# Performance work log

Hardware: AMD Instinct MI355X
Metric: run time of the kernel (lower is better)

The kernel has to match this reference:

```python
import jax, jax.numpy as jnp
import numpy as np

N_NODES = 50000


def _gcn_layer(x, src, dst, norm_src, norm_dst, W, b, act):
    # DGL GraphConv with norm='both': D_out^{-1/2} A D_in^{-1/2} X W + b
    h = x * norm_src[:, None]                      # scale by src out-degree
    m = h[src]                                     # gather messages [E, d]
    agg = jax.ops.segment_sum(m, dst, num_segments=N_NODES)  # scatter-add
    agg = agg * norm_dst[:, None]
    out = agg @ W + b
    if act:
        out = jax.nn.relu(out)
    return out


def setup_inputs() -> dict:
    key = jax.random.key(0)
    ks = jax.random.split(key, 10)
    E = 800000
    in_size, hid, out_size = 128, 128, 64
    features = jax.random.normal(ks[0], (N_NODES, in_size), dtype=jnp.float32)
    src = jax.random.randint(ks[1], (E,), 0, N_NODES, dtype=jnp.int32)
    dst = jax.random.randint(ks[2], (E,), 0, N_NODES, dtype=jnp.int32)
    s = 0.05
    W1 = jax.random.normal(ks[3], (in_size, hid), dtype=jnp.float32) * s
    b1 = jnp.zeros((hid,), dtype=jnp.float32)
    W2 = jax.random.normal(ks[4], (hid, hid), dtype=jnp.float32) * s
    b2 = jnp.zeros((hid,), dtype=jnp.float32)
    W3 = jax.random.normal(ks[5], (hid, out_size), dtype=jnp.float32) * s
    b3 = jnp.zeros((out_size,), dtype=jnp.float32)
    return {"features": features, "W1": W1, "b1": b1, "W2": W2, "b2": b2,
            "W3": W3, "b3": b3, "src": src, "dst": dst}


def reference(features, W1, b1, W2, b2, W3, b3, src, dst):
    ones = jnp.ones(src.shape, dtype=features.dtype)
    out_deg = jax.ops.segment_sum(ones, src, num_segments=N_NODES)
    in_deg = jax.ops.segment_sum(ones, dst, num_segments=N_NODES)
    norm_src = jnp.maximum(out_deg, 1.0) ** -0.5   # clamp(min=1) as in DGL
    norm_dst = jnp.maximum(in_deg, 1.0) ** -0.5
    h = _gcn_layer(features, src, dst, norm_src, norm_dst, W1, b1, act=True)
    # dropout is identity in eval mode
    h = _gcn_layer(h, src, dst, norm_src, norm_dst, W2, b2, act=True)
    h = _gcn_layer(h, src, dst, norm_src, norm_dst, W3, b3, act=False)
    return h
```

## Files before the change

kernel.cpp:

```cpp
#include <hip/hip_runtime.h>
#include <math.h>

#define N_NODES 50000
#define K_DIM 128
#define CAP 64

typedef __attribute__((ext_vector_type(8))) short short8_t;
typedef __attribute__((ext_vector_type(4))) float f32x4_t;
typedef __attribute__((ext_vector_type(8))) _Float16 half8_t;

__device__ inline unsigned short f2bf(float x) {
    unsigned u = __float_as_uint(x);
    unsigned r = u + 0x7fffu + ((u >> 16) & 1u);
    return (unsigned short)(r >> 16);
}
__device__ inline float bf2f(unsigned short h) {
    return __uint_as_float(((unsigned)h) << 16);
}

__global__ __launch_bounds__(256) void prep_kernel(unsigned* __restrict__ cur,
                                                   unsigned* __restrict__ cnt_out,
                                                   _Float16* Yx, _Float16* Yy, _Float16* Yz) {
    int i = blockIdx.x * 256 + threadIdx.x;
    if (i < N_NODES) { cur[i] = 0u; cnt_out[i] = 0u; }
    if (blockIdx.x == 0) {
        int t = threadIdx.x;
        if (t < 128) {
            Yx[(size_t)N_NODES * 128 + t] = (_Float16)0.f;
            Yy[(size_t)N_NODES * 128 + t] = (_Float16)0.f;
        }
        if (t < 64) Yz[(size_t)N_NODES * 64 + t] = (_Float16)0.f;
    }
}

__global__ __launch_bounds__(256) void scatter_count_kernel(const int* __restrict__ src,
                                                            const int* __restrict__ dst, int E,
                                                            unsigned* __restrict__ cnt_out,
                                                            unsigned* __restrict__ cur,
                                                            int* __restrict__ csr) {
    int i = blockIdx.x * 256 + threadIdx.x;
    if (i >= E) return;
    int s = src[i], d = dst[i];
    atomicAdd(&cnt_out[s], 1u);
    unsigned p = atomicAdd(&cur[d], 1u);
    if (p < CAP) csr[((size_t)d << 6) + p] = s;
}

__global__ __launch_bounds__(256) void finalize_kernel(
        const unsigned* __restrict__ cur, const unsigned* __restrict__ cnt_out,
        int* __restrict__ indeg, float* __restrict__ nsrc, float* __restrict__ ndst,
        const float* __restrict__ W1, const float* __restrict__ W2,
        const float* __restrict__ W3,
        unsigned short* __restrict__ W1h, unsigned short* __restrict__ W1l,
        unsigned short* __restrict__ W2h, unsigned short* __restrict__ W2l,
        unsigned short* __restrict__ W3h, unsigned short* __restrict__ W3l) {
    if (blockIdx.x < 196) {
        int v = blockIdx.x * 256 + threadIdx.x;
        if (v >= N_NODES) return;
        unsigned id = cur[v];
        unsigned od = cnt_out[v];
        indeg[v] = (int)(id < CAP ? id : CAP);
        unsigned odc = od < 1u ? 1u : od;
        unsigned idc = id < 1u ? 1u : id;
        nsrc[v] = 1.0f / sqrtf((float)odc);
        ndst[v] = 1.0f / sqrtf((float)idc);
        return;
    }
    int gi = (blockIdx.x - 196) * 256 + threadIdx.x;
    const float* W; unsigned short *WBh, *WBl; int M, i;
    if (gi < 2048)      { W = W1; WBh = W1h; WBl = W1l; M = 128; i = gi; }
    else if (gi < 4096) { W = W2; WBh = W2h; WBl = W2l; M = 128; i = gi - 2048; }
    else if (gi < 5120) { W = W3; WBh = W3h; WBl = W3l; M = 64;  i = gi - 4096; }
    else return;
    int c    = i >> 8;
    int rem  = i & 255;
    int kc   = rem >> 6;
    int lane = rem & 63;
    int m = lane & 15, q = lane >> 4;
    int n = c * 16 + m;
    #pragma unroll
    for (int j = 0; j < 8; ++j) {
        int k = kc * 32 + q * 8 + j;
        float w = W[(size_t)k * M + n];
        unsigned short hi = f2bf(w);
        unsigned short lo = f2bf(w - bf2f(hi));
        WBh[(size_t)i * 8 + j] = hi;
        WBl[(size_t)i * 8 + j] = lo;
    }
}

template <int M>
__global__ __launch_bounds__(256) void gemm_mfma_kernel(
        const float* __restrict__ X,
        const unsigned short* __restrict__ WBh_,
        const unsigned short* __restrict__ WBl_,
        const float* __restrict__ nsrc, _Float16* __restrict__ Yh, int n) {
    constexpr int LSTR = 136;
    __shared__ short Xhi[64 * LSTR];
    __shared__ short Xlo[64 * LSTR];
    int tid = threadIdx.x;
    int lane = tid & 63, wave = tid >> 6;
    int rowBlock = blockIdx.x * 64;

    #pragma unroll
    for (int l = 0; l < 8; ++l) {
        int idx = (tid + l * 256) * 4;
        int r = idx >> 7;
        int c = idx & 127;
        float4 v = make_float4(0.f, 0.f, 0.f, 0.f);
        int gr = rowBlock + r;
        if (gr < n) v = *(const float4*)&X[(size_t)gr * K_DIM + c];
        unsigned short h0 = f2bf(v.x), h1 = f2bf(v.y), h2 = f2bf(v.z), h3 = f2bf(v.w);
        short4 hs = {(short)h0, (short)h1, (short)h2, (short)h3};
        short4 ls = {(short)f2bf(v.x - bf2f(h0)), (short)f2bf(v.y - bf2f(h1)),
                     (short)f2bf(v.z - bf2f(h2)), (short)f2bf(v.w - bf2f(h3))};
        *(short4*)&Xhi[r * LSTR + c] = hs;
        *(short4*)&Xlo[r * LSTR + c] = ls;
    }
    __syncthreads();

    int m = lane & 15, q = lane >> 4;
    short8_t ah[4], al[4];
    {
        int abase = (wave * 16 + m) * LSTR + q * 8;
        #pragma unroll
        for (int kc = 0; kc < 4; ++kc) {
            ah[kc] = *(const short8_t*)&Xhi[abase + kc * 32];
            al[kc] = *(const short8_t*)&Xlo[abase + kc * 32];
        }
    }
    float ns[4];
    int orow0 = rowBlock + wave * 16 + q * 4;
    #pragma unroll
    for (int r = 0; r < 4; ++r) ns[r] = (orow0 + r < n) ? nsrc[orow0 + r] : 0.f;

    const short8_t* WBh = (const short8_t*)WBh_;
    const short8_t* WBl = (const short8_t*)WBl_;
    constexpr int CT = M / 16;
    #pragma unroll
    for (int c = 0; c < CT; ++c) {
        short8_t bh[4], bl[4];
        #pragma unroll
        for (int kc = 0; kc < 4; ++kc) {
            bh[kc] = WBh[(c * 4 + kc) * 64 + lane];
            bl[kc] = WBl[(c * 4 + kc) * 64 + lane];
        }
        f32x4_t acc = {0.f, 0.f, 0.f, 0.f};
        #pragma unroll
        for (int kc = 0; kc < 4; ++kc) {
            acc = __builtin_amdgcn_mfma_f32_16x16x32_bf16(ah[kc], bh[kc], acc, 0, 0, 0);
            acc = __builtin_amdgcn_mfma_f32_16x16x32_bf16(ah[kc], bl[kc], acc, 0, 0, 0);
            acc = __builtin_amdgcn_mfma_f32_16x16x32_bf16(al[kc], bh[kc], acc, 0, 0, 0);
        }
        int col = c * 16 + m;
        #pragma unroll
        for (int r = 0; r < 4; ++r) {
            int row = orow0 + r;
            if (row < n) Yh[(size_t)row * M + col] = (_Float16)(acc[r] * ns[r]);
        }
    }
}

template <int MOUT>
__global__ __launch_bounds__(256, 3) void agg_gemm_kernel(
        const _Float16* __restrict__ Yin,
        const int* __restrict__ indeg, const int* __restrict__ csr,
        const float* __restrict__ ndst, const float* __restrict__ bias,
        const unsigned short* __restrict__ WBh_,
        const unsigned short* __restrict__ WBl_,
        const float* __restrict__ nsrc, _Float16* __restrict__ Yout, int n) {
    constexpr int LSTR = 136;
    __shared__ short Xhi[32 * LSTR];
    __shared__ short Xlo[32 * LSTR];
    int tid = threadIdx.x;
    int lane = tid & 63, wave = tid >> 6;
    int rowBlock = blockIdx.x * 32;

    int sub = tid >> 4;
    int f8  = (tid & 15) * 8;
    #pragma unroll 1
    for (int p = 0; p < 2; ++p) {
        int r = p * 16 + sub;
        int v = rowBlock + r;
        float o[8] = {};
        if (v < n) {
            int deg = indeg[v];
            const int* __restrict__ row = &csr[(size_t)v * CAP];
            float acc[8] = {};
            #pragma unroll 1
            for (int i = 0; i < deg; i += 16) {
                int idx[16];
                #pragma unroll
                for (int t = 0; t < 16; t += 4) {
                    int4 s4 = *(const int4*)&row[i + t];
                    idx[t + 0] = s4.x; idx[t + 1] = s4.y;
                    idx[t + 2] = s4.z; idx[t + 3] = s4.w;
                }
                #pragma unroll
                for (int t = 1; t < 16; ++t)
                    if (i + t >= deg) idx[t] = N_NODES;
                half8_t g[16];
                #pragma unroll
                for (int t = 0; t < 16; ++t)
                    g[t] = *(const half8_t*)&Yin[(size_t)idx[t] * 128 + f8];
                #pragma unroll
                for (int t = 0; t < 16; ++t) {
                    #pragma unroll
                    for (int j = 0; j < 8; ++j) acc[j] += (float)g[t][j];
                }
            }
            float nd = ndst[v];
            #pragma unroll
            for (int j = 0; j < 8; ++j)
                o[j] = fmaxf(nd * acc[j] + bias[f8 + j], 0.f);
        }
        short hs[8], ls[8];
        #pragma unroll
        for (int j = 0; j < 8; ++j) {
            unsigned short h = f2bf(o[j]);
            hs[j] = (short)h;
            ls[j] = (short)f2bf(o[j] - bf2f(h));
        }
        *(short4*)&Xhi[r * LSTR + f8]     = *(short4*)&hs[0];
        *(short4*)&Xhi[r * LSTR + f8 + 4] = *(short4*)&hs[4];
        *(short4*)&Xlo[r * LSTR + f8]     = *(short4*)&ls[0];
        *(short4*)&Xlo[r * LSTR + f8 + 4] = *(short4*)&ls[4];
    }
    __syncthreads();

    int m = lane & 15, q = lane >> 4;
    int wrow = wave & 1;
    int wcol = wave >> 1;
    short8_t ah[4], al[4];
    {
        int abase = (wrow * 16 + m) * LSTR + q * 8;
        #pragma unroll
        for (int kc = 0; kc < 4; ++kc) {
            ah[kc] = *(const short8_t*)&Xhi[abase + kc * 32];
            al[kc] = *(const short8_t*)&Xlo[abase + kc * 32];
        }
    }
    float ns[4];
    int orow0 = rowBlock + wrow * 16 + q * 4;
    #pragma unroll
    for (int r = 0; r < 4; ++r) ns[r] = (orow0 + r < n) ? nsrc[orow0 + r] : 0.f;

    const short8_t* WBh = (const short8_t*)WBh_;
    const short8_t* WBl = (const short8_t*)WBl_;
    constexpr int CTH = MOUT / 32;
    #pragma unroll
    for (int c2 = 0; c2 < CTH; ++c2) {
        int c = wcol * CTH + c2;
        short8_t bh[4], bl[4];
        #pragma unroll
        for (int kc = 0; kc < 4; ++kc) {
            bh[kc] = WBh[(c * 4 + kc) * 64 + lane];
            bl[kc] = WBl[(c * 4 + kc) * 64 + lane];
        }
        f32x4_t acc = {0.f, 0.f, 0.f, 0.f};
        #pragma unroll
        for (int kc = 0; kc < 4; ++kc) {
            acc = __builtin_amdgcn_mfma_f32_16x16x32_bf16(ah[kc], bh[kc], acc, 0, 0, 0);
            acc = __builtin_amdgcn_mfma_f32_16x16x32_bf16(ah[kc], bl[kc], acc, 0, 0, 0);
            acc = __builtin_amdgcn_mfma_f32_16x16x32_bf16(al[kc], bh[kc], acc, 0, 0, 0);
        }
        int col = c * 16 + m;
        #pragma unroll
        for (int r = 0; r < 4; ++r) {
            int row = orow0 + r;
            if (row < n) Yout[(size_t)row * MOUT + col] = (_Float16)(acc[r] * ns[r]);
        }
    }
}

template <int M, bool RELU>
__global__ __launch_bounds__(256, 3) void agg_kernel(const _Float16* __restrict__ Y,
                                                     const int* __restrict__ indeg,
                                                     const int* __restrict__ csr,
                                                     const float* __restrict__ ndst,
                                                     const float* __restrict__ bias,
                                                     float* __restrict__ Z, int n) {
    constexpr int LPN = M / 8;
    constexpr int NPB = 256 / LPN;
    int v = blockIdx.x * NPB + threadIdx.x / LPN;
    if (v >= n) return;
    int f8 = (threadIdx.x % LPN) * 8;
    int deg = indeg[v];
    const int* __restrict__ row = &csr[(size_t)v * CAP];
    float acc[8] = {};
    #pragma unroll 1
    for (int i = 0; i < deg; i += 16) {
        int idx[16];
        #pragma unroll
        for (int t = 0; t < 16; t += 4) {
            int4 s4 = *(const int4*)&row[i + t];
            idx[t + 0] = s4.x; idx[t + 1] = s4.y;
            idx[t + 2] = s4.z; idx[t + 3] = s4.w;
        }
        #pragma unroll
        for (int t = 1; t < 16; ++t)
            if (i + t >= deg) idx[t] = N_NODES;
        half8_t g[16];
        #pragma unroll
        for (int t = 0; t < 16; ++t)
            g[t] = *(const half8_t*)&Y[(size_t)idx[t] * M + f8];
        #pragma unroll
        for (int t = 0; t < 16; ++t) {
            #pragma unroll
            for (int j = 0; j < 8; ++j) acc[j] += (float)g[t][j];
        }
    }
    float nd = ndst[v];
    float4 bb0 = *(const float4*)&bias[f8];
    float4 bb1 = *(const float4*)&bias[f8 + 4];
    float o[8];
    o[0] = nd * acc[0] + bb0.x; o[1] = nd * acc[1] + bb0.y;
    o[2] = nd * acc[2] + bb0.z; o[3] = nd * acc[3] + bb0.w;
    o[4] = nd * acc[4] + bb1.x; o[5] = nd * acc[5] + bb1.y;
    o[6] = nd * acc[6] + bb1.z; o[7] = nd * acc[7] + bb1.w;
    if (RELU) {
        #pragma unroll
        for (int j = 0; j < 8; ++j) o[j] = fmaxf(o[j], 0.f);
    }
    *(float4*)&Z[(size_t)v * M + f8]     = make_float4(o[0], o[1], o[2], o[3]);
    *(float4*)&Z[(size_t)v * M + f8 + 4] = make_float4(o[4], o[5], o[6], o[7]);
}


extern "C" void kernel_launch(void* const* d_in, const int* in_sizes, int n_in,
                              void* d_out, int out_size, void* d_ws, size_t ws_size,
                              hipStream_t stream) {
    const float* features = (const float*)d_in[0];
    const float* W1 = (const float*)d_in[1];
    const float* b1 = (const float*)d_in[2];
    const float* W2 = (const float*)d_in[3];
    const float* b2 = (const float*)d_in[4];
    const float* W3 = (const float*)d_in[5];
    const float* b3 = (const float*)d_in[6];
    const int* src = (const int*)d_in[7];
    const int* dst = (const int*)d_in[8];
    const int E = in_sizes[7];
    const int N = N_NODES;

    char* w = (char*)d_ws;
    auto alloc = [&](size_t bytes) {
        char* p = w;
        w += (bytes + 255) & ~(size_t)255;
        return p;
    };
    _Float16* Yx = (_Float16*)alloc((size_t)(N + 1) * 128 * 2);
    _Float16* Yy = (_Float16*)alloc((size_t)(N + 1) * 128 * 2);
    _Float16* Yz = (_Float16*)alloc((size_t)(N + 1) * 64 * 2);
    int*   csr    = (int*)alloc((size_t)N * CAP * 4);
    unsigned* cnt_out = (unsigned*)alloc((size_t)N * 4);
    unsigned* cur     = (unsigned*)alloc((size_t)N * 4);
    int*   indeg  = (int*)alloc((size_t)N * 4);
    float* nsrc   = (float*)alloc((size_t)N * 4);
    float* ndst   = (float*)alloc((size_t)N * 4);
    unsigned short* W1h = (unsigned short*)alloc(128 * 128 * 2);
    unsigned short* W1l = (unsigned short*)alloc(128 * 128 * 2);
    unsigned short* W2h = (unsigned short*)alloc(128 * 128 * 2);
    unsigned short* W2l = (unsigned short*)alloc(128 * 128 * 2);
    unsigned short* W3h = (unsigned short*)alloc(64 * 128 * 2);
    unsigned short* W3l = (unsigned short*)alloc(64 * 128 * 2);

    prep_kernel<<<196, 256, 0, stream>>>(cur, cnt_out, Yx, Yy, Yz);
    scatter_count_kernel<<<(E + 255) / 256, 256, 0, stream>>>(src, dst, E,
                                                              cnt_out, cur, csr);
    finalize_kernel<<<216, 256, 0, stream>>>(cur, cnt_out, indeg, nsrc, ndst,
                                             W1, W2, W3, W1h, W1l, W2h, W2l, W3h, W3l);

    int gblocks64 = (N + 63) / 64;
    int gblocks32 = (N + 31) / 32;
    gemm_mfma_kernel<128><<<gblocks64, 256, 0, stream>>>(features, W1h, W1l, nsrc, Yx, N);
    agg_gemm_kernel<128><<<gblocks32, 256, 0, stream>>>(Yx, indeg, csr, ndst, b1,
                                                        W2h, W2l, nsrc, Yy, N);
    agg_gemm_kernel<64><<<gblocks32, 256, 0, stream>>>(Yy, indeg, csr, ndst, b2,
                                                       W3h, W3l, nsrc, Yz, N);
    agg_kernel<64, false><<<(N + 31) / 32, 256, 0, stream>>>(Yz, indeg, csr, ndst, b3,
                                                             (float*)d_out, N);
}
```

Baseline: 258.4 us.

## Slice-partitioned CSR build with 16-bit indices and fused degree normalization

Replaces the scatter/count plus finalize kernels with a single build kernel. Each of 8 block groups reads the whole edge list with vectorized int4 loads but only performs atomics for nodes in its own 6250-node slice, which is meant to localize atomic traffic. CSR neighbour indices are stored as 16-bit values, halving the index footprint, and the normalization factors are recomputed inline from the raw counts, which removes the finalize kernel and the indeg/nsrc/ndst arrays. The costs are reading src/dst eight times and truncating node ids above 65535 (N is 50000, so they fit).

```diff
diff --git a/kernel.cpp b/kernel.cpp
--- a/kernel.cpp
+++ b/kernel.cpp
@@ -4,8 +4,10 @@
 #define N_NODES 50000
 #define K_DIM 128
 #define CAP 64
+#define SLICE 6250
 
 typedef __attribute__((ext_vector_type(8))) short short8_t;
+typedef __attribute__((ext_vector_type(8))) unsigned short ushort8_t;
 typedef __attribute__((ext_vector_type(4))) float f32x4_t;
 typedef __attribute__((ext_vector_type(8))) _Float16 half8_t;
 
@@ -17,56 +19,34 @@
 __device__ inline float bf2f(unsigned short h) {
     return __uint_as_float(((unsigned)h) << 16);
 }
-
-__global__ __launch_bounds__(256) void prep_kernel(unsigned* __restrict__ cur,
-                                                   unsigned* __restrict__ cnt_out,
-                                                   _Float16* Yx, _Float16* Yy, _Float16* Yz) {
-    int i = blockIdx.x * 256 + threadIdx.x;
-    if (i < N_NODES) { cur[i] = 0u; cnt_out[i] = 0u; }
-    if (blockIdx.x == 0) {
-        int t = threadIdx.x;
-        if (t < 128) {
-            Yx[(size_t)N_NODES * 128 + t] = (_Float16)0.f;
-            Yy[(size_t)N_NODES * 128 + t] = (_Float16)0.f;
-        }
-        if (t < 64) Yz[(size_t)N_NODES * 64 + t] = (_Float16)0.f;
-    }
-}
-
-__global__ __launch_bounds__(256) void scatter_count_kernel(const int* __restrict__ src,
-                                                            const int* __restrict__ dst, int E,
-                                                            unsigned* __restrict__ cnt_out,
-                                                            unsigned* __restrict__ cur,
-                                                            int* __restrict__ csr) {
-    int i = blockIdx.x * 256 + threadIdx.x;
-    if (i >= E) return;
-    int s = src[i], d = dst[i];
-    atomicAdd(&cnt_out[s], 1u);
-    unsigned p = atomicAdd(&cur[d], 1u);
-    if (p < CAP) csr[((size_t)d << 6) + p] = s;
-}
-
-__global__ __launch_bounds__(256) void finalize_kernel(
-        const unsigned* __restrict__ cur, const unsigned* __restrict__ cnt_out,
-        int* __restrict__ indeg, float* __restrict__ nsrc, float* __restrict__ ndst,
+__device__ inline float invsqrt_deg(unsigned d) {
+    unsigned c = d < 1u ? 1u : d;
+    return 1.0f / sqrtf((float)c);
+}
+
+__global__ __launch_bounds__(256) void prep_kernel(
+        unsigned* __restrict__ cnt,
+        _Float16* Yx, _Float16* Yy, _Float16* Yz,
         const float* __restrict__ W1, const float* __restrict__ W2,
         const float* __restrict__ W3,
         unsigned short* __restrict__ W1h, unsigned short* __restrict__ W1l,
         unsigned short* __restrict__ W2h, unsigned short* __restrict__ W2l,
         unsigned short* __restrict__ W3h, unsigned short* __restrict__ W3l) {
-    if (blockIdx.x < 196) {
-        int v = blockIdx.x * 256 + threadIdx.x;
-        if (v >= N_NODES) return;
-        unsigned id = cur[v];
-        unsigned od = cnt_out[v];
-        indeg[v] = (int)(id < CAP ? id : CAP);
-        unsigned odc = od < 1u ? 1u : od;
-        unsigned idc = id < 1u ? 1u : id;
-        nsrc[v] = 1.0f / sqrtf((float)odc);
-        ndst[v] = 1.0f / sqrtf((float)idc);
+    int b = blockIdx.x, tid = threadIdx.x;
+    if (b < 391) {
+        int i = b * 256 + tid;
+        if (i < 2 * N_NODES) cnt[i] = 0u;
         return;
     }
-    int gi = (blockIdx.x - 196) * 256 + threadIdx.x;
+    if (b == 391) {
+        if (tid < 128) {
+            Yx[(size_t)N_NODES * 128 + tid] = (_Float16)0.f;
+            Yy[(size_t)N_NODES * 128 + tid] = (_Float16)0.f;
+        }
+        if (tid < 64) Yz[(size_t)N_NODES * 64 + tid] = (_Float16)0.f;
+        return;
+    }
+    int gi = (b - 392) * 256 + tid;
     const float* W; unsigned short *WBh, *WBl; int M, i;
     if (gi < 2048)      { W = W1; WBh = W1h; WBl = W1l; M = 128; i = gi; }
     else if (gi < 4096) { W = W2; WBh = W2h; WBl = W2l; M = 128; i = gi - 2048; }
@@ -89,12 +69,49 @@
     }
 }
 
+__global__ __launch_bounds__(256) void build_kernel(const int* __restrict__ src,
+                                                    const int* __restrict__ dst, int E,
+                                                    unsigned* __restrict__ cnt_out,
+                                                    unsigned* __restrict__ cur,
+                                                    unsigned short* __restrict__ csr) {
+    int g = blockIdx.x & 7;
+    int k = blockIdx.x >> 3;
+    int per = ((E + 63) / 64 + 3) & ~3;
+    int start = k * per;
+    int end = start + per; if (end > E) end = E;
+    int slo = g * SLICE;
+    for (int i = start + threadIdx.x * 4; i < end; i += 256 * 4) {
+        int4 s4, d4;
+        if (i + 4 <= end) {
+            s4 = *(const int4*)&src[i];
+            d4 = *(const int4*)&dst[i];
+        } else {
+            s4 = make_int4(-1, -1, -1, -1); d4 = s4;
+            for (int j = 0; i + j < end; ++j) {
+                ((int*)&s4)[j] = src[i + j];
+                ((int*)&d4)[j] = dst[i + j];
+            }
+        }
+        #pragma unroll
+        for (int j = 0; j < 4; ++j) {
+            int s = ((int*)&s4)[j];
+            int d = ((int*)&d4)[j];
+            if (s < 0) continue;
+            if ((unsigned)(s - slo) < (unsigned)SLICE) atomicAdd(&cnt_out[s], 1u);
+            if ((unsigned)(d - slo) < (unsigned)SLICE) {
+                unsigned p = atomicAdd(&cur[d], 1u);
+                if (p < CAP) csr[((size_t)d << 6) + p] = (unsigned short)s;
+            }
+        }
+    }
+}
+
 template <int M>
 __global__ __launch_bounds__(256) void gemm_mfma_kernel(
         const float* __restrict__ X,
         const unsigned short* __restrict__ WBh_,
         const unsigned short* __restrict__ WBl_,
-        const float* __restrict__ nsrc, _Float16* __restrict__ Yh, int n) {
+        const unsigned* __restrict__ cnt_out, _Float16* __restrict__ Yh, int n) {
     constexpr int LSTR = 136;
     __shared__ short Xhi[64 * LSTR];
     __shared__ short Xlo[64 * LSTR];
@@ -132,7 +149,8 @@
     float ns[4];
     int orow0 = rowBlock + wave * 16 + q * 4;
     #pragma unroll
-    for (int r = 0; r < 4; ++r) ns[r] = (orow0 + r < n) ? nsrc[orow0 + r] : 0.f;
+    for (int r = 0; r < 4; ++r)
+        ns[r] = (orow0 + r < n) ? invsqrt_deg(cnt_out[orow0 + r]) : 0.f;
 
     const short8_t* WBh = (const short8_t*)WBh_;
     const short8_t* WBl = (const short8_t*)WBl_;
@@ -164,11 +182,12 @@
 template <int MOUT>
 __global__ __launch_bounds__(256, 3) void agg_gemm_kernel(
         const _Float16* __restrict__ Yin,
-        const int* __restrict__ indeg, const int* __restrict__ csr,
-        const float* __restrict__ ndst, const float* __restrict__ bias,
+        const unsigned* __restrict__ cur, const unsigned* __restrict__ cnt_out,
+        const unsigned short* __restrict__ csr,
+        const float* __restrict__ bias,
         const unsigned short* __restrict__ WBh_,
         const unsigned short* __restrict__ WBl_,
-        const float* __restrict__ nsrc, _Float16* __restrict__ Yout, int n) {
+        _Float16* __restrict__ Yout, int n) {
     constexpr int LSTR = 136;
     __shared__ short Xhi[32 * LSTR];
     __shared__ short Xlo[32 * LSTR];
@@ -184,18 +203,19 @@
         int v = rowBlock + r;
         float o[8] = {};
         if (v < n) {
-            int deg = indeg[v];
-            const int* __restrict__ row = &csr[(size_t)v * CAP];
+            unsigned idv = cur[v];
+            int deg = idv < CAP ? (int)idv : CAP;
+            const unsigned short* __restrict__ row = &csr[(size_t)v * CAP];
             float acc[8] = {};
             #pragma unroll 1
             for (int i = 0; i < deg; i += 16) {
+                ushort8_t ia = *(const ushort8_t*)&row[i];
+                ushort8_t ib = *(const ushort8_t*)&row[i + 8];
                 int idx[16];
                 #pragma unroll
-                for (int t = 0; t < 16; t += 4) {
-                    int4 s4 = *(const int4*)&row[i + t];
-                    idx[t + 0] = s4.x; idx[t + 1] = s4.y;
-                    idx[t + 2] = s4.z; idx[t + 3] = s4.w;
-                }
+                for (int t = 0; t < 8; ++t) idx[t] = (int)ia[t];
+                #pragma unroll
+                for (int t = 0; t < 8; ++t) idx[8 + t] = (int)ib[t];
                 #pragma unroll
                 for (int t = 1; t < 16; ++t)
                     if (i + t >= deg) idx[t] = N_NODES;
@@ -209,7 +229,7 @@
                     for (int j = 0; j < 8; ++j) acc[j] += (float)g[t][j];
                 }
             }
-            float nd = ndst[v];
+            float nd = invsqrt_deg(idv);
             #pragma unroll
             for (int j = 0; j < 8; ++j)
                 o[j] = fmaxf(nd * acc[j] + bias[f8 + j], 0.f);
@@ -243,7 +263,8 @@
     float ns[4];
     int orow0 = rowBlock + wrow * 16 + q * 4;
     #pragma unroll
-    for (int r = 0; r < 4; ++r) ns[r] = (orow0 + r < n) ? nsrc[orow0 + r] : 0.f;
+    for (int r = 0; r < 4; ++r)
+        ns[r] = (orow0 + r < n) ? invsqrt_deg(cnt_out[orow0 + r]) : 0.f;
 
     const short8_t* WBh = (const short8_t*)WBh_;
     const short8_t* WBl = (const short8_t*)WBl_;
@@ -275,9 +296,8 @@
 
 template <int M, bool RELU>
 __global__ __launch_bounds__(256, 3) void agg_kernel(const _Float16* __restrict__ Y,
-                                                     const int* __restrict__ indeg,
-                                                     const int* __restrict__ csr,
-                                                     const float* __restrict__ ndst,
+                                                     const unsigned* __restrict__ cur,
+                                                     const unsigned short* __restrict__ csr,
                                                      const float* __restrict__ bias,
                                                      float* __restrict__ Z, int n) {
     constexpr int LPN = M / 8;
@@ -285,18 +305,19 @@
     int v = blockIdx.x * NPB + threadIdx.x / LPN;
     if (v >= n) return;
     int f8 = (threadIdx.x % LPN) * 8;
-    int deg = indeg[v];
-    const int* __restrict__ row = &csr[(size_t)v * CAP];
+    unsigned idv = cur[v];
+    int deg = idv < CAP ? (int)idv : CAP;
+    const unsigned short* __restrict__ row = &csr[(size_t)v * CAP];
     float acc[8] = {};
     #pragma unroll 1
     for (int i = 0; i < deg; i += 16) {
+        ushort8_t ia = *(const ushort8_t*)&row[i];
+        ushort8_t ib = *(const ushort8_t*)&row[i + 8];
         int idx[16];
         #pragma unroll
-        for (int t = 0; t < 16; t += 4) {
-            int4 s4 = *(const int4*)&row[i + t];
-            idx[t + 0] = s4.x; idx[t + 1] = s4.y;
-            idx[t + 2] = s4.z; idx[t + 3] = s4.w;
-        }
+        for (int t = 0; t < 8; ++t) idx[t] = (int)ia[t];
+        #pragma unroll
+        for (int t = 0; t < 8; ++t) idx[8 + t] = (int)ib[t];
         #pragma unroll
         for (int t = 1; t < 16; ++t)
             if (i + t >= deg) idx[t] = N_NODES;
@@ -310,7 +331,7 @@
             for (int j = 0; j < 8; ++j) acc[j] += (float)g[t][j];
         }
     }
-    float nd = ndst[v];
+    float nd = invsqrt_deg(idv);
     float4 bb0 = *(const float4*)&bias[f8];
     float4 bb1 = *(const float4*)&bias[f8 + 4];
     float o[8];
@@ -351,12 +372,10 @@
     _Float16* Yx = (_Float16*)alloc((size_t)(N + 1) * 128 * 2);
     _Float16* Yy = (_Float16*)alloc((size_t)(N + 1) * 128 * 2);
     _Float16* Yz = (_Float16*)alloc((size_t)(N + 1) * 64 * 2);
-    int*   csr    = (int*)alloc((size_t)N * CAP * 4);
-    unsigned* cnt_out = (unsigned*)alloc((size_t)N * 4);
-    unsigned* cur     = (unsigned*)alloc((size_t)N * 4);
-    int*   indeg  = (int*)alloc((size_t)N * 4);
-    float* nsrc   = (float*)alloc((size_t)N * 4);
-    float* ndst   = (float*)alloc((size_t)N * 4);
+    unsigned short* csr = (unsigned short*)alloc((size_t)N * CAP * 2);
+    unsigned* cnt = (unsigned*)alloc((size_t)2 * N * 4);
+    unsigned* cnt_out = cnt;
+    unsigned* cur     = cnt + N;
     unsigned short* W1h = (unsigned short*)alloc(128 * 128 * 2);
     unsigned short* W1l = (unsigned short*)alloc(128 * 128 * 2);
     unsigned short* W2h = (unsigned short*)alloc(128 * 128 * 2);
@@ -364,19 +383,17 @@
     unsigned short* W3h = (unsigned short*)alloc(64 * 128 * 2);
     unsigned short* W3l = (unsigned short*)alloc(64 * 128 * 2);
 
-    prep_kernel<<<196, 256, 0, stream>>>(cur, cnt_out, Yx, Yy, Yz);
-    scatter_count_kernel<<<(E + 255) / 256, 256, 0, stream>>>(src, dst, E,
-                                                              cnt_out, cur, csr);
-    finalize_kernel<<<216, 256, 0, stream>>>(cur, cnt_out, indeg, nsrc, ndst,
-                                             W1, W2, W3, W1h, W1l, W2h, W2l, W3h, W3l);
+    prep_kernel<<<412, 256, 0, stream>>>(cnt, Yx, Yy, Yz,
+                                         W1, W2, W3, W1h, W1l, W2h, W2l, W3h, W3l);
+    build_kernel<<<512, 256, 0, stream>>>(src, dst, E, cnt_out, cur, csr);
 
     int gblocks64 = (N + 63) / 64;
     int gblocks32 = (N + 31) / 32;
-    gemm_mfma_kernel<128><<<gblocks64, 256, 0, stream>>>(features, W1h, W1l, nsrc, Yx, N);
-    agg_gemm_kernel<128><<<gblocks32, 256, 0, stream>>>(Yx, indeg, csr, ndst, b1,
-                                                        W2h, W2l, nsrc, Yy, N);
-    agg_gemm_kernel<64><<<gblocks32, 256, 0, stream>>>(Yy, indeg, csr, ndst, b2,
-                                                       W3h, W3l, nsrc, Yz, N);
-    agg_kernel<64, false><<<(N + 31) / 32, 256, 0, stream>>>(Yz, indeg, csr, ndst, b3,
-                                                             (float*)d_out, N);
-}
+    gemm_mfma_kernel<128><<<gblocks64, 256, 0, stream>>>(features, W1h, W1l, cnt_out, Yx, N);
+    agg_gemm_kernel<128><<<gblocks32, 256, 0, stream>>>(Yx, cur, cnt_out, csr, b1,
+                                                        W2h, W2l, Yy, N);
+    agg_gemm_kernel<64><<<gblocks32, 256, 0, stream>>>(Yy, cur, cnt_out, csr, b2,
+                                                       W3h, W3l, Yz, N);
+    agg_kernel<64, false><<<gblocks32, 256, 0, stream>>>(Yz, cur, csr, b3,
+                                                         (float*)d_out, N);
+}
```

After: 269.2 us. 1.04x slower.
